# Kernel optimization log

Measured on AMD Instinct MI355X. Metric: run time of the kernel, lower is better.

## Reference

```python
import jax, jax.numpy as jnp
import numpy as np

S, B, D, H, DK, DFF, L, P = 128, 16, 512, 8, 64, 2048, 4, 4096


def setup_inputs() -> dict:
    key = jax.random.key(0)
    ks = jax.random.split(key, 10)
    def rn(k, shape, scale=0.02):
        return jax.random.normal(k, shape, jnp.float32) * scale
    return dict(
        x_seq=jax.random.normal(ks[0], (S, B, D), jnp.float32),
        w_query=rn(ks[1], (L, D, H * DK)),
        query_pos_bias=rn(ks[2], (L, H, DK)),
        key_pos_emb=rn(ks[3], (L, P, H, DK)),
        w_out=rn(ks[4], (L, D, D)), b_out=jnp.zeros((L, D), jnp.float32),
        ln1_g=jnp.ones((L, D), jnp.float32), ln1_b=jnp.zeros((L, D), jnp.float32),
        ln2_g=jnp.ones((L, D), jnp.float32), ln2_b=jnp.zeros((L, D), jnp.float32),
        w_ff1=rn(ks[5], (L, D, DFF)), b_ff1=jnp.zeros((L, DFF), jnp.float32),
        w_ff2=rn(ks[6], (L, DFF, D)), b_ff2=jnp.zeros((L, D), jnp.float32),
        norm_g=jnp.ones((D,), jnp.float32), norm_b=jnp.zeros((D,), jnp.float32),
        comb_w=jnp.ones((L + 1,), jnp.float32),
        w_key=rn(ks[7], (D, H * DK)), w_value=rn(ks[8], (D, H * DK)),
    )


def _layer_norm(x, g, b, eps=1e-5):
    mu = jnp.mean(x, -1, keepdims=True)
    var = jnp.mean((x - mu) ** 2, -1, keepdims=True)
    return (x - mu) * jax.lax.rsqrt(var + eps) * g + b


def reference(x_seq, w_query, query_pos_bias, key_pos_emb, w_out, b_out,
              ln1_g, ln1_b, ln2_g, ln2_b, w_ff1, b_ff1, w_ff2, b_ff2,
              norm_g, norm_b, comb_w, w_key, w_value):
    scale = 1.0 / jnp.sqrt(jnp.float32(DK))
    comb = jax.nn.softmax(comb_w)           # softmax over n_layers+1 weights
    jpos = jnp.arange(S)

    def step(carry, inp):
        mem_k, mem_v = carry                # [S, B, H, DK] growing KV memory stack
        x, t = inp                          # x: [B, D], t: scalar step index
        # valid memory slots are steps 0..t-1 (at t==0 attention is gated off below)
        valid = (jpos < jnp.maximum(t, 1))[:, None, None]   # [S,1,1]
        outs = [x]
        for l in range(L):
            # --- FeedbackAttention (pre-LN, relative key position embeddings) ---
            z = _layer_norm(x, ln1_g[l], ln1_b[l])
            q = (z @ w_query[l]).reshape(B, H, DK)
            # original: key_pos_embeddings[-t:]  ->  table index P - t + j for slot j
            kpe = jnp.take(key_pos_emb[l], jnp.clip(P - t + jpos, 0, P - 1), axis=0)  # [S,H,DK]
            ac = jnp.einsum('bhd,jbhd->jbh', q + query_pos_bias[l], mem_k)
            bd = jnp.einsum('bhd,jhd->jbh', q, kpe)
            scores = jnp.where(valid, (ac + bd) * scale, -1e9)
            attn = jax.nn.softmax(scores, axis=0)             # softmax over memory dim
            av = jnp.einsum('jbh,jbhd->bhd', attn, mem_v).reshape(B, D)
            x = jnp.where(t > 0, x + av @ w_out[l] + b_out[l], x)
            # --- FeedForward (pre-LN, ReLU) ---
            z = _layer_norm(x, ln2_g[l], ln2_b[l])
            x = x + jax.nn.relu(z @ w_ff1[l] + b_ff1[l]) @ w_ff2[l] + b_ff2[l]
            outs.append(x)
        # softmax-weighted combination of [input + layer outputs]
        mem = jnp.einsum('lbd,l->bd', jnp.stack(outs), comb)
        mem_k = mem_k.at[t].set((mem @ w_key).reshape(B, H, DK))
        mem_v = mem_v.at[t].set((mem @ w_value).reshape(B, H, DK))
        return (mem_k, mem_v), x

    mem0 = jnp.zeros((S, B, H, DK), x_seq.dtype)
    _, res = jax.lax.scan(jax.checkpoint(step), (mem0, mem0), (x_seq, jnp.arange(S)))
    return _layer_norm(res, norm_g, norm_b)
```

## Files before the change

kernel.cpp:

```cpp
#include <hip/hip_runtime.h>


#define S_ 128
#define B_ 16
#define D_ 512
#define H_ 8
#define DK_ 64
#define DFF_ 2048
#define L_ 4
#define P_ 4096

#define NBLK 128
#define NTHR 1024

struct FtkvParams {
  const float *x_seq, *w_query, *qpb, *kpe, *w_out, *b_out;
  const float *ln1_g, *ln1_b, *ln2_g, *ln2_b;
  const float *w_ff1, *b_ff1, *w_ff2, *b_ff2;
  const float *norm_g, *norm_b, *comb_w, *w_key, *w_value;
  float *out;
  float *dpart;
  float *dpart2;
  unsigned *memK;
  unsigned *memV;
  const uint4 *wqp;
  const uint4 *wop;
  const uint4 *w1p;
  const uint4 *w2p;
  const uint4 *wkp;
  const uint4 *wvp;
  unsigned int *bar;
};

__device__ __forceinline__ float cload(const float *p_) {
  return __hip_atomic_load(p_, __ATOMIC_RELAXED, __HIP_MEMORY_SCOPE_AGENT);
}
__device__ __forceinline__ void cstore(float *p_, float v) {
  __hip_atomic_store(p_, v, __ATOMIC_RELAXED, __HIP_MEMORY_SCOPE_AGENT);
}

__device__ __forceinline__ float waveRedSum(float v) {
#pragma unroll
  for (int off = 32; off; off >>= 1) v += __shfl_xor(v, off, 64);
  return v;
}
__device__ __forceinline__ float waveRedMax(float v) {
#pragma unroll
  for (int off = 32; off; off >>= 1) v = fmaxf(v, __shfl_xor(v, off, 64));
  return v;
}

#define UNPK(w, flo, fhi)                                     \
  float flo = __uint_as_float((unsigned)(w) << 16);           \
  float fhi = __uint_as_float((unsigned)(w) & 0xffff0000u);

__device__ __forceinline__ float dot8(const float *z, uint4 w) {
  UNPK(w.x, a0, a1); UNPK(w.y, b0, b1);
  UNPK(w.z, c0, c1); UNPK(w.w, d0, d1);
  return ((z[0] * a0 + z[1] * a1) + (z[2] * b0 + z[3] * b1)) +
         ((z[4] * c0 + z[5] * c1) + (z[6] * d0 + z[7] * d1));
}

__device__ __forceinline__ void gbarN(unsigned *arr, unsigned &epoch,
                                      unsigned n) {
  __syncthreads();
  const unsigned e = ++epoch;
  if (threadIdx.x == 0) {
    __hip_atomic_fetch_add(arr, 1u, __ATOMIC_RELAXED,
                           __HIP_MEMORY_SCOPE_AGENT);
    while (__hip_atomic_load(arr, __ATOMIC_RELAXED,
                             __HIP_MEMORY_SCOPE_AGENT) < e * n)
      __builtin_amdgcn_s_sleep(1);
  }
  __syncthreads();
}

__global__ void ftkv_init(unsigned *bar) {
  for (int i = threadIdx.x; i < 4096; i += 256) bar[i] = 0u;
}

__device__ __forceinline__ unsigned bf16rne(float x) {
  unsigned b = __float_as_uint(x);
  return (b + 0x7fffu + ((b >> 16) & 1u)) >> 16;
}

__global__ void ftkv_pack(const float *src, unsigned *dst, int K, int N) {
  int total = (K / 2) * N;
  int n4 = N * 4;
  for (int i = blockIdx.x * blockDim.x + threadIdx.x; i < total;
       i += gridDim.x * blockDim.x) {
    int k8 = i / n4, rem = i - k8 * n4;
    int col = rem >> 2, q = rem & 3;
    int r0 = 8 * k8 + 2 * q;
    dst[i] = bf16rne(src[(size_t)r0 * N + col]) |
             (bf16rne(src[(size_t)(r0 + 1) * N + col]) << 16);
  }
}

#define LNSTATS(val, mu_, rs_)                                             \
  {                                                                        \
    __syncthreads();                                                       \
    if (tid < 512) {                                                       \
      float _s1 = waveRedSum(val), _s2 = waveRedSum((val) * (val));        \
      if (lane == 0) { sRed[wid] = _s1; sRed[8 + wid] = _s2; }             \
    }                                                                      \
    __syncthreads();                                                       \
    if (tid == 0) {                                                        \
      float _a = 0.f, _c = 0.f;                                            \
      for (int _i = 0; _i < 8; ++_i) { _a += sRed[_i]; _c += sRed[8 + _i];}\
      float _mu = _a * (1.f / 512.f);                                      \
      float _var = _c * (1.f / 512.f) - _mu * _mu;                         \
      sRed[16] = _mu; sRed[17] = rsqrtf(_var + 1e-5f);                     \
    }                                                                      \
    __syncthreads();                                                       \
    mu_ = sRed[16]; rs_ = sRed[17];                                        \
  }

__global__ __launch_bounds__(NTHR, 4) void ftkv_main(FtkvParams p) {
  const int bid = blockIdx.x;
  const int tid = threadIdx.x;
  const int lane = tid & 63, wid = tid >> 6;
  const int g = bid >> 3;
  const int cs = bid & 7;

  __shared__ float sZ[512];
  __shared__ float sP[1024];
  __shared__ float sH[256];
  __shared__ float sQ[64], sQB[64], sS[128], sRed[20];

  unsigned *garr = p.bar + g * 32;
  unsigned gep = 0;

  float cw0 = p.comb_w[0], cw1 = p.comb_w[1], cw2 = p.comb_w[2],
        cw3 = p.comb_w[3], cw4 = p.comb_w[4];
  float cm = fmaxf(fmaxf(fmaxf(cw0, cw1), fmaxf(cw2, cw3)), cw4);
  float e0 = __expf(cw0 - cm), e1 = __expf(cw1 - cm), e2 = __expf(cw2 - cm),
        e3 = __expf(cw3 - cm), e4 = __expf(cw4 - cm);
  float einv = 1.0f / (e0 + e1 + e2 + e3 + e4);
  float comb0 = e0 * einv, comb1 = e1 * einv, comb2 = e2 * einv,
        comb3 = e3 * einv, comb4 = e4 * einv;

  float xr = 0.f, mr = 0.f;
  if (tid < 512) {
    xr = p.x_seq[g * D_ + tid];
    mr = comb0 * xr;
  }

  unsigned *memKb = p.memK + ((size_t)(g * H_ + cs)) * S_ * 32;
  unsigned *memVb = p.memV + ((size_t)(g * H_ + cs)) * S_ * 32;

  for (int t = 0; t < S_; ++t) {
    for (int l = 0; l < L_; ++l) {
      if (l > 0 && tid < 512) {
        float s = p.b_ff2[(l - 1) * D_ + tid];
#pragma unroll
        for (int c2 = 0; c2 < 8; ++c2)
          s += cload(&p.dpart2[((size_t)g * 8 + c2) * D_ + tid]);
        xr += s;
        const float cl = (l == 1) ? comb1 : (l == 2) ? comb2 : comb3;
        mr += cl * xr;
      }

      if (t > 0) {
        float mu, rs;
        LNSTATS(xr, mu, rs);
        if (tid < 512)
          sZ[tid] = (xr - mu) * rs * p.ln1_g[l * D_ + tid] +
                    p.ln1_b[l * D_ + tid];
        __syncthreads();
        {
          int d = tid & 63, ks = tid >> 6;
          const uint4 *wq = p.wqp + (size_t)l * 64 * 512 + cs * 64 + d;
          float acc = 0.f;
#pragma unroll
          for (int j = 0; j < 4; ++j) {
            int k8 = ks * 4 + j;
            acc += dot8(&sZ[8 * k8], wq[(size_t)k8 * 512]);
          }
          sP[tid] = acc;
        }
        __syncthreads();
        if (tid < 64) {
          float q = 0.f;
#pragma unroll
          for (int ks = 0; ks < 16; ++ks) q += sP[ks * 64 + tid];
          sQ[tid] = q;
          sQB[tid] = q + p.qpb[(l * H_ + cs) * 64 + tid];
        }
        __syncthreads();
        {
          int j = tid & 127, ds = tid >> 7;
          float acc = 0.f;
          if (j < t) {
            uint4 mku = ((const uint4 *)(memKb + (size_t)j * 32))[ds];
            const float4 *kp = (const float4 *)(p.kpe +
                (((size_t)l * P_ + (P_ - t + j)) * H_ + cs) * 64 + ds * 8);
            float4 b0 = kp[0], b1 = kp[1];
            UNPK(mku.x, k0, k1); UNPK(mku.y, k2, k3);
            UNPK(mku.z, k4, k5); UNPK(mku.w, k6, k7);
            const float *qb = &sQB[ds * 8], *qr = &sQ[ds * 8];
            acc = (qb[0] * k0 + qb[1] * k1 + qb[2] * k2 + qb[3] * k3) +
                  (qb[4] * k4 + qb[5] * k5 + qb[6] * k6 + qb[7] * k7) +
                  (qr[0] * b0.x + qr[1] * b0.y + qr[2] * b0.z + qr[3] * b0.w) +
                  (qr[4] * b1.x + qr[5] * b1.y + qr[6] * b1.z + qr[7] * b1.w);
          }
          sP[tid] = acc;
        }
        __syncthreads();
        if (tid < 128) {
          float sc = ((sP[tid] + sP[tid + 128]) + (sP[tid + 256] + sP[tid + 384])) +
                     ((sP[tid + 512] + sP[tid + 640]) + (sP[tid + 768] + sP[tid + 896]));
          sS[tid] = (tid < t) ? sc * 0.125f : -1e30f;
        }
        __syncthreads();
        if (tid < 64) {
          float m = waveRedMax(fmaxf(sS[tid], sS[tid + 64]));
          if (tid == 0) sRed[18] = m;
        }
        __syncthreads();
        if (tid < 128)
          sS[tid] = (tid < t) ? __expf(sS[tid] - sRed[18]) : 0.f;
        __syncthreads();
        if (tid < 64) {
          float s = waveRedSum(sS[tid] + sS[tid + 64]);
          if (tid == 0) sRed[19] = s;
        }
        __syncthreads();
        {
          int d = tid & 63, js = tid >> 6;
          int j0 = js * 8, j1 = (j0 + 8 < t) ? (j0 + 8) : t;
          float acc = 0.f;
          const ushort *mv = (const ushort *)memVb;
          for (int j = j0; j < j1; ++j) {
            float vv = __uint_as_float(((unsigned)mv[(size_t)j * 64 + d]) << 16);
            acc += sS[j] * vv;
          }
          sP[tid] = acc;
        }
        __syncthreads();
        if (tid < 64) {
          float a = 0.f;
#pragma unroll
          for (int js = 0; js < 16; ++js) a += sP[js * 64 + tid];
          sQ[tid] = a / sRed[19];
        }
        __syncthreads();
        {
          int col = tid & 511, ks = tid >> 9;
          const uint4 *wo = p.wop + (size_t)l * 64 * 512 + col;
          float acc = 0.f;
#pragma unroll
          for (int j = 0; j < 4; ++j) {
            int k8l = ks * 4 + j;
            acc += dot8(&sQ[8 * k8l], wo[(size_t)(cs * 8 + k8l) * 512]);
          }
          sP[tid] = acc;
        }
        __syncthreads();
        if (tid < 512)
          cstore(&p.dpart[((size_t)g * 8 + cs) * D_ + tid],
                 sP[tid] + sP[512 + tid]);
        gbarN(garr, gep, 8);
      }

      if (t > 0 && tid < 512) {
        float s = p.b_out[l * D_ + tid];
#pragma unroll
        for (int c2 = 0; c2 < 8; ++c2)
          s += cload(&p.dpart[((size_t)g * 8 + c2) * D_ + tid]);
        xr += s;
      }
      {
        float mu, rs;
        LNSTATS(xr, mu, rs);
        if (tid < 512)
          sZ[tid] = (xr - mu) * rs * p.ln2_g[l * D_ + tid] +
                    p.ln2_b[l * D_ + tid];
      }
      __syncthreads();
      {
        int c = tid & 255, ks = tid >> 8;
        const uint4 *w1 = p.w1p + (size_t)l * 64 * DFF_ + cs * 256 + c;
        float acc = 0.f;
#pragma unroll 8
        for (int j = 0; j < 16; ++j) {
          int k8 = ks * 16 + j;
          acc += dot8(&sZ[8 * k8], w1[(size_t)k8 * DFF_]);
        }
        sP[tid] = acc;
      }
      __syncthreads();
      if (tid < 256) {
        float h = ((sP[tid] + sP[256 + tid]) + (sP[512 + tid] + sP[768 + tid])) +
                  p.b_ff1[l * DFF_ + cs * 256 + tid];
        sH[tid] = fmaxf(h, 0.f);
      }
      __syncthreads();
      {
        int col = tid & 511, ks = tid >> 9;
        const uint4 *w2 = p.w2p + (size_t)l * 256 * 512 + col;
        float acc = 0.f;
#pragma unroll 8
        for (int j = 0; j < 16; ++j) {
          int k8l = ks * 16 + j;
          acc += dot8(&sH[8 * k8l], w2[(size_t)(cs * 32 + k8l) * 512]);
        }
        sP[tid] = acc;
      }
      __syncthreads();
      if (tid < 512)
        cstore(&p.dpart2[((size_t)g * 8 + cs) * D_ + tid],
               sP[tid] + sP[512 + tid]);
      gbarN(garr, gep, 8);
    }

    if (tid < 512) {
      float s = p.b_ff2[3 * D_ + tid];
#pragma unroll
      for (int c2 = 0; c2 < 8; ++c2)
        s += cload(&p.dpart2[((size_t)g * 8 + c2) * D_ + tid]);
      xr += s;
      mr += comb4 * xr;
      sZ[tid] = mr;
    }
    __syncthreads();
    {
      int kv = tid >> 9, r = tid & 511, d = r & 63, ks = r >> 6;
      const uint4 *w4 = (kv ? p.wvp : p.wkp) + cs * 64 + d;
      float acc = 0.f;
#pragma unroll
      for (int j = 0; j < 8; ++j) {
        int k8 = ks * 8 + j;
        acc += dot8(&sZ[8 * k8], w4[(size_t)k8 * 512]);
      }
      sP[tid] = acc;
    }
    __syncthreads();
    if (tid < 128) {
      int kv = tid >> 6, d = tid & 63;
      float v = 0.f;
#pragma unroll
      for (int ks = 0; ks < 8; ++ks) v += sP[kv * 512 + ks * 64 + d];
      sS[tid] = v;
    }
    __syncthreads();
    if (tid < 64) {
      int kv = tid >> 5, d2 = tid & 31;
      float lo = sS[kv * 64 + 2 * d2], hi = sS[kv * 64 + 2 * d2 + 1];
      unsigned pk = bf16rne(lo) | (bf16rne(hi) << 16);
      unsigned *dst = kv ? memVb : memKb;
      dst[(size_t)t * 32 + d2] = pk;
    }
    {
      float mu, rs;
      LNSTATS(xr, mu, rs);
      if (tid < 512 && (tid >> 6) == cs)
        p.out[((size_t)t * B_ + g) * D_ + tid] =
            (xr - mu) * rs * p.norm_g[tid] + p.norm_b[tid];
    }
    if (t + 1 < S_ && tid < 512) {
      xr = p.x_seq[((size_t)(t + 1) * B_ + g) * D_ + tid];
      mr = comb0 * xr;
    }
  }
}

extern "C" void kernel_launch(void *const *d_in, const int *in_sizes, int n_in,
                              void *d_out, int out_size, void *d_ws,
                              size_t ws_size, hipStream_t stream) {
  (void)in_sizes; (void)n_in; (void)out_size; (void)ws_size;

  FtkvParams p;
  p.x_seq  = (const float *)d_in[0];
  p.w_query = (const float *)d_in[1];
  p.qpb    = (const float *)d_in[2];
  p.kpe    = (const float *)d_in[3];
  p.w_out  = (const float *)d_in[4];
  p.b_out  = (const float *)d_in[5];
  p.ln1_g  = (const float *)d_in[6];
  p.ln1_b  = (const float *)d_in[7];
  p.ln2_g  = (const float *)d_in[8];
  p.ln2_b  = (const float *)d_in[9];
  p.w_ff1  = (const float *)d_in[10];
  p.b_ff1  = (const float *)d_in[11];
  p.w_ff2  = (const float *)d_in[12];
  p.b_ff2  = (const float *)d_in[13];
  p.norm_g = (const float *)d_in[14];
  p.norm_b = (const float *)d_in[15];
  p.comb_w = (const float *)d_in[16];
  p.w_key  = (const float *)d_in[17];
  p.w_value = (const float *)d_in[18];
  p.out = (float *)d_out;

  char *ws = (char *)d_ws;
  p.bar = (unsigned int *)ws;
  float *f = (float *)(ws + 16384);
  p.dpart  = f; f += B_ * 8 * D_;
  p.dpart2 = f; f += B_ * 8 * D_;
  unsigned *u = (unsigned *)f;
  p.memK = u; u += B_ * H_ * S_ * 32;
  p.memV = u; u += B_ * H_ * S_ * 32;
  unsigned *wqp = u; u += L_ * 256 * 512;
  unsigned *wop = u; u += L_ * 256 * 512;
  unsigned *w1p = u; u += L_ * 256 * DFF_;
  unsigned *w2p = u; u += L_ * 1024 * 512;
  unsigned *wkp = u; u += 256 * 512;
  unsigned *wvp = u; u += 256 * 512;
  p.wqp = (const uint4 *)wqp; p.wop = (const uint4 *)wop;
  p.w1p = (const uint4 *)w1p; p.w2p = (const uint4 *)w2p;
  p.wkp = (const uint4 *)wkp; p.wvp = (const uint4 *)wvp;

  ftkv_init<<<dim3(1), dim3(256), 0, stream>>>(p.bar);
  for (int l = 0; l < L_; ++l) {
    ftkv_pack<<<dim3(256), dim3(256), 0, stream>>>(
        p.w_query + (size_t)l * 512 * 512, wqp + (size_t)l * 256 * 512, 512, 512);
    ftkv_pack<<<dim3(256), dim3(256), 0, stream>>>(
// ... 11 lines not shown
```

Baseline: 14.26 ms.

## Assign block roles by XCC id so column slices share an XCD

Result: no change. 14.43 ms (+1.2%).

```diff
diff --git a/kernel.cpp b/kernel.cpp
--- a/kernel.cpp
+++ b/kernel.cpp
@@ -38,6 +38,9 @@
 __device__ __forceinline__ void cstore(float *p_, float v) {
   __hip_atomic_store(p_, v, __ATOMIC_RELAXED, __HIP_MEMORY_SCOPE_AGENT);
 }
+__device__ __forceinline__ unsigned aload(const unsigned *p_) {
+  return __hip_atomic_load(p_, __ATOMIC_RELAXED, __HIP_MEMORY_SCOPE_AGENT);
+}
 
 __device__ __forceinline__ float waveRedSum(float v) {
 #pragma unroll
@@ -117,16 +120,50 @@
   }
 
 __global__ __launch_bounds__(NTHR, 4) void ftkv_main(FtkvParams p) {
-  const int bid = blockIdx.x;
   const int tid = threadIdx.x;
   const int lane = tid & 63, wid = tid >> 6;
-  const int g = bid >> 3;
-  const int cs = bid & 7;
 
   __shared__ float sZ[512];
   __shared__ float sP[1024];
   __shared__ float sH[256];
   __shared__ float sQ[64], sQB[64], sS[128], sRed[20];
+  __shared__ int sAssign[2];
+
+  if (tid == 0) {
+    unsigned x;
+    asm volatile("s_getreg_b32 %0, hwreg(HW_REG_XCC_ID)" : "=s"(x));
+    x &= 7u;
+    unsigned *cnt = p.bar + 2048;
+    unsigned n = __hip_atomic_fetch_add(&cnt[x * 32], 1u, __ATOMIC_RELAXED,
+                                        __HIP_MEMORY_SCOPE_AGENT);
+    int mycs, myg;
+    if (n < 16u) {
+      mycs = (int)x;
+      myg = (int)n;
+    } else {
+      for (;;) {
+        unsigned s = 0;
+        for (int i = 0; i < 8; ++i) s += aload(&cnt[i * 32]);
+        if (s >= (unsigned)NBLK) break;
+        __builtin_amdgcn_s_sleep(8);
+      }
+      unsigned e = __hip_atomic_fetch_add(&cnt[256], 1u, __ATOMIC_RELAXED,
+                                          __HIP_MEMORY_SCOPE_AGENT);
+      mycs = 0; myg = 0;
+      for (int c = 0; c < 8; ++c) {
+        unsigned cc = aload(&cnt[c * 32]);
+        unsigned used = cc < 16u ? cc : 16u;
+        unsigned u = 16u - used;
+        if (e < u) { mycs = c; myg = (int)(used + e); break; }
+        e -= u;
+      }
+    }
+    sAssign[0] = mycs;
+    sAssign[1] = myg;
+  }
+  __syncthreads();
+  const int cs = sAssign[0];
+  const int g = sAssign[1];
 
   unsigned *garr = p.bar + g * 32;
   unsigned gep = 0;
```

## Interleave two batch groups per block with split arrive/wait barriers

Applied to the files above, without the earlier changes.

New measurement: 26.99 ms. 1.89x slower.

```diff
diff --git a/kernel.cpp b/kernel.cpp
--- a/kernel.cpp
+++ b/kernel.cpp
@@ -10,7 +10,7 @@
 #define L_ 4
 #define P_ 4096
 
-#define NBLK 128
+#define NBLK 64
 #define NTHR 1024
 
 struct FtkvParams {
@@ -61,15 +61,17 @@
          ((z[4] * c0 + z[5] * c1) + (z[6] * d0 + z[7] * d1));
 }
 
-__device__ __forceinline__ void gbarN(unsigned *arr, unsigned &epoch,
-                                      unsigned n) {
-  __syncthreads();
-  const unsigned e = ++epoch;
-  if (threadIdx.x == 0) {
+__device__ __forceinline__ void arrive(unsigned *arr, unsigned &ep) {
+  __syncthreads();
+  if (threadIdx.x == 0)
     __hip_atomic_fetch_add(arr, 1u, __ATOMIC_RELAXED,
                            __HIP_MEMORY_SCOPE_AGENT);
+  ++ep;
+}
+__device__ __forceinline__ void waitbar(unsigned *arr, unsigned ep) {
+  if (threadIdx.x == 0) {
     while (__hip_atomic_load(arr, __ATOMIC_RELAXED,
-                             __HIP_MEMORY_SCOPE_AGENT) < e * n)
+                             __HIP_MEMORY_SCOPE_AGENT) < ep * 8u)
       __builtin_amdgcn_s_sleep(1);
   }
   __syncthreads();
@@ -97,39 +99,247 @@
   }
 }
 
-#define LNSTATS(val, mu_, rs_)                                             \
-  {                                                                        \
-    __syncthreads();                                                       \
-    if (tid < 512) {                                                       \
-      float _s1 = waveRedSum(val), _s2 = waveRedSum((val) * (val));        \
-      if (lane == 0) { sRed[wid] = _s1; sRed[8 + wid] = _s2; }             \
-    }                                                                      \
-    __syncthreads();                                                       \
-    if (tid == 0) {                                                        \
-      float _a = 0.f, _c = 0.f;                                            \
-      for (int _i = 0; _i < 8; ++_i) { _a += sRed[_i]; _c += sRed[8 + _i];}\
-      float _mu = _a * (1.f / 512.f);                                      \
-      float _var = _c * (1.f / 512.f) - _mu * _mu;                         \
-      sRed[16] = _mu; sRed[17] = rsqrtf(_var + 1e-5f);                     \
-    }                                                                      \
-    __syncthreads();                                                       \
-    mu_ = sRed[16]; rs_ = sRed[17];                                        \
-  }
+__device__ __forceinline__ void lnstats(int tid, int lane, int wid, float v,
+                                        float *sRed, float &mu, float &rs) {
+  __syncthreads();
+  if (tid < 512) {
+    float s1 = waveRedSum(v), s2 = waveRedSum(v * v);
+    if (lane == 0) { sRed[wid] = s1; sRed[8 + wid] = s2; }
+  }
+  __syncthreads();
+  float a = 0.f, c = 0.f;
+#pragma unroll
+  for (int i = 0; i < 8; ++i) { a += sRed[i]; c += sRed[8 + i]; }
+  mu = a * (1.f / 512.f);
+  float var = c * (1.f / 512.f) - mu * mu;
+  rs = rsqrtf(var + 1e-5f);
+}
+
+struct Smem {
+  float sZ[512];
+  float sP[1024];
+  float sH[256];
+  float sQ[64], sQB[64], sS[128], sRed[20];
+};
+
+__device__ __forceinline__ void bodyA(const FtkvParams &p, Smem &sm, int tid,
+                                      int lane, int wid, int t, int l, int g,
+                                      int cs, float xr, unsigned *memKb,
+                                      unsigned *memVb) {
+  float mu, rs;
+  lnstats(tid, lane, wid, xr, sm.sRed, mu, rs);
+  if (tid < 512)
+    sm.sZ[tid] = (xr - mu) * rs * p.ln1_g[l * D_ + tid] +
+                 p.ln1_b[l * D_ + tid];
+  __syncthreads();
+  {
+    int d = tid & 63, ks = tid >> 6;
+    const uint4 *wq = p.wqp + (size_t)l * 64 * 512 + cs * 64 + d;
+    float acc = 0.f;
+#pragma unroll
+    for (int j = 0; j < 4; ++j) {
+      int k8 = ks * 4 + j;
+      acc += dot8(&sm.sZ[8 * k8], wq[(size_t)k8 * 512]);
+    }
+    sm.sP[tid] = acc;
+  }
+  __syncthreads();
+  if (tid < 64) {
+    float q = 0.f;
+#pragma unroll
+    for (int ks = 0; ks < 16; ++ks) q += sm.sP[ks * 64 + tid];
+    sm.sQ[tid] = q;
+    sm.sQB[tid] = q + p.qpb[(l * H_ + cs) * 64 + tid];
+  }
+  __syncthreads();
+  {
+    int j = tid & 127, ds = tid >> 7;
+    float acc = 0.f;
+    if (j < t) {
+      uint4 mku = ((const uint4 *)(memKb + (size_t)j * 32))[ds];
+      const float4 *kp = (const float4 *)(p.kpe +
+          (((size_t)l * P_ + (P_ - t + j)) * H_ + cs) * 64 + ds * 8);
+      float4 b0 = kp[0], b1 = kp[1];
+      UNPK(mku.x, k0, k1); UNPK(mku.y, k2, k3);
+      UNPK(mku.z, k4, k5); UNPK(mku.w, k6, k7);
+      const float *qb = &sm.sQB[ds * 8], *qr = &sm.sQ[ds * 8];
+      acc = (qb[0] * k0 + qb[1] * k1 + qb[2] * k2 + qb[3] * k3) +
+            (qb[4] * k4 + qb[5] * k5 + qb[6] * k6 + qb[7] * k7) +
+            (qr[0] * b0.x + qr[1] * b0.y + qr[2] * b0.z + qr[3] * b0.w) +
+            (qr[4] * b1.x + qr[5] * b1.y + qr[6] * b1.z + qr[7] * b1.w);
+    }
+    sm.sP[tid] = acc;
+  }
+  __syncthreads();
+  if (tid < 128) {
+    float sc =
+        ((sm.sP[tid] + sm.sP[tid + 128]) + (sm.sP[tid + 256] + sm.sP[tid + 384])) +
+        ((sm.sP[tid + 512] + sm.sP[tid + 640]) + (sm.sP[tid + 768] + sm.sP[tid + 896]));
+    sm.sS[tid] = (tid < t) ? sc * 0.125f : -1e30f;
+  }
+  __syncthreads();
+  if (tid < 64) {
+    float m = waveRedMax(fmaxf(sm.sS[tid], sm.sS[tid + 64]));
+    if (tid == 0) sm.sRed[18] = m;
+  }
+  __syncthreads();
+  if (tid < 128)
+    sm.sS[tid] = (tid < t) ? __expf(sm.sS[tid] - sm.sRed[18]) : 0.f;
+  __syncthreads();
+  if (tid < 64) {
+    float s = waveRedSum(sm.sS[tid] + sm.sS[tid + 64]);
+    if (tid == 0) sm.sRed[19] = s;
+  }
+  __syncthreads();
+  {
+    int d = tid & 63, js = tid >> 6;
+    int j0 = js * 8, j1 = (j0 + 8 < t) ? (j0 + 8) : t;
+    float acc = 0.f;
+    const ushort *mv = (const ushort *)memVb;
+    for (int j = j0; j < j1; ++j) {
+      float vv = __uint_as_float(((unsigned)mv[(size_t)j * 64 + d]) << 16);
+      acc += sm.sS[j] * vv;
+    }
+    sm.sP[tid] = acc;
+  }
+  __syncthreads();
+  if (tid < 64) {
+    float a = 0.f;
+#pragma unroll
+    for (int js = 0; js < 16; ++js) a += sm.sP[js * 64 + tid];
+    sm.sQ[tid] = a / sm.sRed[19];
+  }
+  __syncthreads();
+  {
+    int col = tid & 511, ks = tid >> 9;
+    const uint4 *wo = p.wop + (size_t)l * 64 * 512 + col;
+    float acc = 0.f;
+#pragma unroll
+    for (int j = 0; j < 4; ++j) {
+      int k8l = ks * 4 + j;
+      acc += dot8(&sm.sQ[8 * k8l], wo[(size_t)(cs * 8 + k8l) * 512]);
+    }
+    sm.sP[tid] = acc;
+  }
+  __syncthreads();
+  if (tid < 512)
+    cstore(&p.dpart[((size_t)g * 8 + cs) * D_ + tid],
+           sm.sP[tid] + sm.sP[512 + tid]);
+}
+
+__device__ __forceinline__ void bodyB(const FtkvParams &p, Smem &sm, int tid,
+                                      int lane, int wid, int l, int g, int cs,
+                                      float xr) {
+  float mu, rs;
+  lnstats(tid, lane, wid, xr, sm.sRed, mu, rs);
+  if (tid < 512)
+    sm.sZ[tid] = (xr - mu) * rs * p.ln2_g[l * D_ + tid] +
+                 p.ln2_b[l * D_ + tid];
+  __syncthreads();
+  {
+    int c = tid & 255, ks = tid >> 8;
+    const uint4 *w1 = p.w1p + (size_t)l * 64 * DFF_ + cs * 256 + c;
+    float acc = 0.f;
+#pragma unroll 8
+    for (int j = 0; j < 16; ++j) {
+      int k8 = ks * 16 + j;
+      acc += dot8(&sm.sZ[8 * k8], w1[(size_t)k8 * DFF_]);
+    }
+    sm.sP[tid] = acc;
+  }
+  __syncthreads();
+  if (tid < 256) {
+    float h = ((sm.sP[tid] + sm.sP[256 + tid]) +
+               (sm.sP[512 + tid] + sm.sP[768 + tid])) +
+              p.b_ff1[l * DFF_ + cs * 256 + tid];
+    sm.sH[tid] = fmaxf(h, 0.f);
+  }
+  __syncthreads();
+  {
+    int col = tid & 511, ks = tid >> 9;
+    const uint4 *w2 = p.w2p + (size_t)l * 256 * 512 + col;
+    float acc = 0.f;
+#pragma unroll 8
+    for (int j = 0; j < 16; ++j) {
+      int k8l = ks * 16 + j;
+      acc += dot8(&sm.sH[8 * k8l], w2[(size_t)(cs * 32 + k8l) * 512]);
+    }
+    sm.sP[tid] = acc;
+  }
+  __syncthreads();
+  if (tid < 512)
+    cstore(&p.dpart2[((size_t)g * 8 + cs) * D_ + tid],
+           sm.sP[tid] + sm.sP[512 + tid]);
+}
+
+__device__ __forceinline__ void bodyE(const FtkvParams &p, Smem &sm, int tid,
+                                      int lane, int wid, int t, int g, int cs,
+                                      float &xr, float &mr, float comb0,
+                                      float comb4, unsigned *memKb,
+                                      unsigned *memVb) {
+  if (tid < 512) {
+    float s = p.b_ff2[3 * D_ + tid];
+#pragma unroll
+    for (int c2 = 0; c2 < 8; ++c2)
+      s += cload(&p.dpart2[((size_t)g * 8 + c2) * D_ + tid]);
+    xr += s;
+    mr += comb4 * xr;
+    sm.sZ[tid] = mr;
+  }
+  __syncthreads();
+  {
+    int kv = tid >> 9, r = tid & 511, d = r & 63, ks = r >> 6;
+    const uint4 *w4 = (kv ? p.wvp : p.wkp) + cs * 64 + d;
+    float acc = 0.f;
+#pragma unroll
+    for (int j = 0; j < 8; ++j) {
+      int k8 = ks * 8 + j;
+      acc += dot8(&sm.sZ[8 * k8], w4[(size_t)k8 * 512]);
+    }
+    sm.sP[tid] = acc;
+  }
+  __syncthreads();
+  if (tid < 128) {
+    int kv = tid >> 6, d = tid & 63;
+    float v = 0.f;
+#pragma unroll
+    for (int ks = 0; ks < 8; ++ks) v += sm.sP[kv * 512 + ks * 64 + d];
+    sm.sS[tid] = v;
+  }
+  __syncthreads();
+  if (tid < 64) {
+    int kv = tid >> 5, d2 = tid & 31;
+    float lo = sm.sS[kv * 64 + 2 * d2], hi = sm.sS[kv * 64 + 2 * d2 + 1];
+    unsigned pk = bf16rne(lo) | (bf16rne(hi) << 16);
+    unsigned *dst = kv ? memVb : memKb;
+    dst[(size_t)t * 32 + d2] = pk;
+  }
+  {
+    float mu, rs;
+    lnstats(tid, lane, wid, xr, sm.sRed, mu, rs);
+    if (tid < 512 && (tid >> 6) == cs)
+      p.out[((size_t)t * B_ + g) * D_ + tid] =
+          (xr - mu) * rs * p.norm_g[tid] + p.norm_b[tid];
+  }
+  if (t + 1 < S_ && tid < 512) {
+    xr = p.x_seq[((size_t)(t + 1) * B_ + g) * D_ + tid];
+    mr = comb0 * xr;
+  }
+}
 
 __global__ __launch_bounds__(NTHR, 4) void ftkv_main(FtkvParams p) {
   const int bid = blockIdx.x;
   const int tid = threadIdx.x;
   const int lane = tid & 63, wid = tid >> 6;
-  const int g = bid >> 3;
+  const int gp = bid >> 3;
   const int cs = bid & 7;
 
-  __shared__ float sZ[512];
-  __shared__ float sP[1024];
-  __shared__ float sH[256];
-  __shared__ float sQ[64], sQB[64], sS[128], sRed[20];
-
-  unsigned *garr = p.bar + g * 32;
-  unsigned gep = 0;
+  __shared__ Smem sm;
+
+  const int gA = gp, gB = gp + 8;
+  unsigned *arrA = p.bar + gA * 32;
+  unsigned *arrB = p.bar + gB * 32;
+  unsigned epA = 0, epB = 0;
 
   float cw0 = p.comb_w[0], cw1 = p.comb_w[1], cw2 = p.comb_w[2],
         cw3 = p.comb_w[3], cw4 = p.comb_w[4];
@@ -140,228 +350,102 @@
   float comb0 = e0 * einv, comb1 = e1 * einv, comb2 = e2 * einv,
         comb3 = e3 * einv, comb4 = e4 * einv;
 
-  float xr = 0.f, mr = 0.f;
+  float xrA = 0.f, mrA = 0.f, xrB = 0.f, mrB = 0.f;
   if (tid < 512) {
-    xr = p.x_seq[g * D_ + tid];
-    mr = comb0 * xr;
-  }
-
-  unsigned *memKb = p.memK + ((size_t)(g * H_ + cs)) * S_ * 32;
-  unsigned *memVb = p.memV + ((size_t)(g * H_ + cs)) * S_ * 32;
+    xrA = p.x_seq[gA * D_ + tid];
+    mrA = comb0 * xrA;
+    xrB = p.x_seq[gB * D_ + tid];
+    mrB = comb0 * xrB;
+  }
+
+  unsigned *memKbA = p.memK + ((size_t)(gA * H_ + cs)) * S_ * 32;
+  unsigned *memVbA = p.memV + ((size_t)(gA * H_ + cs)) * S_ * 32;
+  unsigned *memKbB = p.memK + ((size_t)(gB * H_ + cs)) * S_ * 32;
+  unsigned *memVbB = p.memV + ((size_t)(gB * H_ + cs)) * S_ * 32;
 
   for (int t = 0; t < S_; ++t) {
     for (int l = 0; l < L_; ++l) {
-      if (l > 0 && tid < 512) {
-        float s = p.b_ff2[(l - 1) * D_ + tid];
-#pragma unroll
-        for (int c2 = 0; c2 < 8; ++c2)
-          s += cload(&p.dpart2[((size_t)g * 8 + c2) * D_ + tid]);
-        xr += s;
-        const float cl = (l == 1) ? comb1 : (l == 2) ? comb2 : comb3;
-        mr += cl * xr;
+      const float cl = (l == 1) ? comb1 : (l == 2) ? comb2 : comb3;
+
+      if (t > 0) {
+        waitbar(arrA, epA);
+        if (l > 0 && tid < 512) {
+          float s = p.b_ff2[(l - 1) * D_ + tid];
+#pragma unroll
+          for (int c2 = 0; c2 < 8; ++c2)
+            s += cload(&p.dpart2[((size_t)gA * 8 + c2) * D_ + tid]);
+          xrA += s;
+          mrA += cl * xrA;
+        }
+        bodyA(p, sm, tid, lane, wid, t, l, gA, cs, xrA, memKbA, memVbA);
+        arrive(arrA, epA);
+
+        waitbar(arrB, epB);
+        if (l > 0 && tid < 512) {
+          float s = p.b_ff2[(l - 1) * D_ + tid];
+#pragma unroll
+          for (int c2 = 0; c2 < 8; ++c2)
+            s += cload(&p.dpart2[((size_t)gB * 8 + c2) * D_ + tid]);
+          xrB += s;
+          mrB += cl * xrB;
+        }
+        bodyA(p, sm, tid, lane, wid, t, l, gB, cs, xrB, memKbB, memVbB);
+        arrive(arrB, epB);
+
+        waitbar(arrA, epA);
+        if (tid < 512) {
+          float s = p.b_out[l * D_ + tid];
+#pragma unroll
+          for (int c2 = 0; c2 < 8; ++c2)
+            s += cload(&p.dpart[((size_t)gA * 8 + c2) * D_ + tid]);
+          xrA += s;
+        }
+        bodyB(p, sm, tid, lane, wid, l, gA, cs, xrA);
+        arrive(arrA, epA);
+
+        waitbar(arrB, epB);
+        if (tid < 512) {
+          float s = p.b_out[l * D_ + tid];
+#pragma unroll
+          for (int c2 = 0; c2 < 8; ++c2)
+            s += cload(&p.dpart[((size_t)gB * 8 + c2) * D_ + tid]);
+          xrB += s;
+        }
+        bodyB(p, sm, tid, lane, wid, l, gB, cs, xrB);
+        arrive(arrB, epB);
+      } else {
+        waitbar(arrA, epA);
+        if (l > 0 && tid < 512) {
+          float s = p.b_ff2[(l - 1) * D_ + tid];
+#pragma unroll
+          for (int c2 = 0; c2 < 8; ++c2)
+            s += cload(&p.dpart2[((size_t)gA * 8 + c2) * D_ + tid]);
+          xrA += s;
+          mrA += cl * xrA;
+        }
+        bodyB(p, sm, tid, lane, wid, l, gA, cs, xrA);
+        arrive(arrA, epA);
+
+        waitbar(arrB, epB);
+        if (l > 0 && tid < 512) {
+          float s = p.b_ff2[(l - 1) * D_ + tid];
+#pragma unroll
+          for (int c2 = 0; c2 < 8; ++c2)
+            s += cload(&p.dpart2[((size_t)gB * 8 + c2) * D_ + tid]);
+          xrB += s;
+          mrB += cl * xrB;
+        }
+        bodyB(p, sm, tid, lane, wid, l, gB, cs, xrB);
+        arrive(arrB, epB);
       }
-
-      if (t > 0) {
-        float mu, rs;
-        LNSTATS(xr, mu, rs);
-        if (tid < 512)
-          sZ[tid] = (xr - mu) * rs * p.ln1_g[l * D_ + tid] +
-                    p.ln1_b[l * D_ + tid];
-        __syncthreads();
-        {
-          int d = tid & 63, ks = tid >> 6;
-          const uint4 *wq = p.wqp + (size_t)l * 64 * 512 + cs * 64 + d;
-          float acc = 0.f;
-#pragma unroll
-          for (int j = 0; j < 4; ++j) {
-            int k8 = ks * 4 + j;
-            acc += dot8(&sZ[8 * k8], wq[(size_t)k8 * 512]);
-          }
-          sP[tid] = acc;
-        }
-        __syncthreads();
-        if (tid < 64) {
-          float q = 0.f;
-#pragma unroll
-          for (int ks = 0; ks < 16; ++ks) q += sP[ks * 64 + tid];
-          sQ[tid] = q;
-          sQB[tid] = q + p.qpb[(l * H_ + cs) * 64 + tid];
-        }
-        __syncthreads();
-        {
-          int j = tid & 127, ds = tid >> 7;
-          float acc = 0.f;
-          if (j < t) {
-            uint4 mku = ((const uint4 *)(memKb + (size_t)j * 32))[ds];
-            const float4 *kp = (const float4 *)(p.kpe +
-                (((size_t)l * P_ + (P_ - t + j)) * H_ + cs) * 64 + ds * 8);
-            float4 b0 = kp[0], b1 = kp[1];
-            UNPK(mku.x, k0, k1); UNPK(mku.y, k2, k3);
-            UNPK(mku.z, k4, k5); UNPK(mku.w, k6, k7);
-            const float *qb = &sQB[ds * 8], *qr = &sQ[ds * 8];
-            acc = (qb[0] * k0 + qb[1] * k1 + qb[2] * k2 + qb[3] * k3) +
-                  (qb[4] * k4 + qb[5] * k5 + qb[6] * k6 + qb[7] * k7) +
-                  (qr[0] * b0.x + qr[1] * b0.y + qr[2] * b0.z + qr[3] * b0.w) +
-                  (qr[4] * b1.x + qr[5] * b1.y + qr[6] * b1.z + qr[7] * b1.w);
-          }
-          sP[tid] = acc;
-        }
-        __syncthreads();
-        if (tid < 128) {
-          float sc = ((sP[tid] + sP[tid + 128]) + (sP[tid + 256] + sP[tid + 384])) +
-                     ((sP[tid + 512] + sP[tid + 640]) + (sP[tid + 768] + sP[tid + 896]));
-          sS[tid] = (tid < t) ? sc * 0.125f : -1e30f;
-        }
-        __syncthreads();
-        if (tid < 64) {
-          float m = waveRedMax(fmaxf(sS[tid], sS[tid + 64]));
-          if (tid == 0) sRed[18] = m;
-        }
-        __syncthreads();
-        if (tid < 128)
-          sS[tid] = (tid < t) ? __expf(sS[tid] - sRed[18]) : 0.f;
-        __syncthreads();
-        if (tid < 64) {
-          float s = waveRedSum(sS[tid] + sS[tid + 64]);
-          if (tid == 0) sRed[19] = s;
-        }
-        __syncthreads();
-        {
-          int d = tid & 63, js = tid >> 6;
-          int j0 = js * 8, j1 = (j0 + 8 < t) ? (j0 + 8) : t;
-          float acc = 0.f;
-          const ushort *mv = (const ushort *)memVb;
-          for (int j = j0; j < j1; ++j) {
-            float vv = __uint_as_float(((unsigned)mv[(size_t)j * 64 + d]) << 16);
-            acc += sS[j] * vv;
-          }
-          sP[tid] = acc;
-        }
-        __syncthreads();
-        if (tid < 64) {
-          float a = 0.f;
-#pragma unroll
-          for (int js = 0; js < 16; ++js) a += sP[js * 64 + tid];
-          sQ[tid] = a / sRed[19];
-        }
-        __syncthreads();
-        {
-          int col = tid & 511, ks = tid >> 9;
-          const uint4 *wo = p.wop + (size_t)l * 64 * 512 + col;
-          float acc = 0.f;
-#pragma unroll
-          for (int j = 0; j < 4; ++j) {
-            int k8l = ks * 4 + j;
-            acc += dot8(&sQ[8 * k8l], wo[(size_t)(cs * 8 + k8l) * 512]);
-          }
-          sP[tid] = acc;
-        }
-        __syncthreads();
-        if (tid < 512)
-          cstore(&p.dpart[((size_t)g * 8 + cs) * D_ + tid],
-                 sP[tid] + sP[512 + tid]);
-        gbarN(garr, gep, 8);
-      }
-
-      if (t > 0 && tid < 512) {
-        float s = p.b_out[l * D_ + tid];
-#pragma unroll
-        for (int c2 = 0; c2 < 8; ++c2)
-          s += cload(&p.dpart[((size_t)g * 8 + c2) * D_ + tid]);
-        xr += s;
-      }
-      {
-        float mu, rs;
-        LNSTATS(xr, mu, rs);
-        if (tid < 512)
-          sZ[tid] = (xr - mu) * rs * p.ln2_g[l * D_ + tid] +
-                    p.ln2_b[l * D_ + tid];
-      }
-      __syncthreads();
-      {
-        int c = tid & 255, ks = tid >> 8;
-        const uint4 *w1 = p.w1p + (size_t)l * 64 * DFF_ + cs * 256 + c;
-        float acc = 0.f;
-#pragma unroll 8
-        for (int j = 0; j < 16; ++j) {
-          int k8 = ks * 16 + j;
-          acc += dot8(&sZ[8 * k8], w1[(size_t)k8 * DFF_]);
-        }
-        sP[tid] = acc;
-      }
-      __syncthreads();
-      if (tid < 256) {
-        float h = ((sP[tid] + sP[256 + tid]) + (sP[512 + tid] + sP[768 + tid])) +
-                  p.b_ff1[l * DFF_ + cs * 256 + tid];
-        sH[tid] = fmaxf(h, 0.f);
-      }
-      __syncthreads();
-      {
-        int col = tid & 511, ks = tid >> 9;
-        const uint4 *w2 = p.w2p + (size_t)l * 256 * 512 + col;
-        float acc = 0.f;
-#pragma unroll 8
-        for (int j = 0; j < 16; ++j) {
-          int k8l = ks * 16 + j;
-          acc += dot8(&sH[8 * k8l], w2[(size_t)(cs * 32 + k8l) * 512]);
-        }
-        sP[tid] = acc;
-      }
-      __syncthreads();
-      if (tid < 512)
-        cstore(&p.dpart2[((size_t)g * 8 + cs) * D_ + tid],
-               sP[tid] + sP[512 + tid]);
-      gbarN(garr, gep, 8);
-    }
-
-    if (tid < 512) {
-      float s = p.b_ff2[3 * D_ + tid];
-#pragma unroll
-      for (int c2 = 0; c2 < 8; ++c2)
-        s += cload(&p.dpart2[((size_t)g * 8 + c2) * D_ + tid]);
-      xr += s;
-      mr += comb4 * xr;
-      sZ[tid] = mr;
-    }
-    __syncthreads();
-    {
-      int kv = tid >> 9, r = tid & 511, d = r & 63, ks = r >> 6;
-      const uint4 *w4 = (kv ? p.wvp : p.wkp) + cs * 64 + d;
-      float acc = 0.f;
-#pragma unroll
-      for (int j = 0; j < 8; ++j) {
-        int k8 = ks * 8 + j;
-        acc += dot8(&sZ[8 * k8], w4[(size_t)k8 * 512]);
-      }
-      sP[tid] = acc;
-    }
-    __syncthreads();
-    if (tid < 128) {
-      int kv = tid >> 6, d = tid & 63;
-      float v = 0.f;
-#pragma unroll
-      for (int ks = 0; ks < 8; ++ks) v += sP[kv * 512 + ks * 64 + d];
-      sS[tid] = v;
-    }
-    __syncthreads();
-    if (tid < 64) {
-      int kv = tid >> 5, d2 = tid & 31;
-      float lo = sS[kv * 64 + 2 * d2], hi = sS[kv * 64 + 2 * d2 + 1];
-      unsigned pk = bf16rne(lo) | (bf16rne(hi) << 16);
-      unsigned *dst = kv ? memVb : memKb;
-      dst[(size_t)t * 32 + d2] = pk;
-    }
-    {
-      float mu, rs;
-      LNSTATS(xr, mu, rs);
-      if (tid < 512 && (tid >> 6) == cs)
-        p.out[((size_t)t * B_ + g) * D_ + tid] =
-            (xr - mu) * rs * p.norm_g[tid] + p.norm_b[tid];
-    }
-    if (t + 1 < S_ && tid < 512) {
-      xr = p.x_seq[((size_t)(t + 1) * B_ + g) * D_ + tid];
-      mr = comb0 * xr;
-    }
+    }
+
+    waitbar(arrA, epA);
+    bodyE(p, sm, tid, lane, wid, t, gA, cs, xrA, mrA, comb0, comb4, memKbA,
+          memVbA);
+    waitbar(arrB, epB);
+    bodyE(p, sm, tid, lane, wid, t, gB, cs, xrB, mrB, comb0, comb4, memKbB,
+          memVbB);
   }
 }
 
```

## Prefetch weights into registers before LN barriers and use LDS-only barriers

Applied to the files above, without the earlier changes.

New measurement: 11.66 ms. 18.2% less time.

```diff
diff --git a/kernel.cpp b/kernel.cpp
--- a/kernel.cpp
+++ b/kernel.cpp
@@ -50,6 +50,11 @@
   return v;
 }
 
+__device__ __forceinline__ void lbar() {
+  asm volatile("s_waitcnt lgkmcnt(0)" ::: "memory");
+  __builtin_amdgcn_s_barrier();
+}
+
 #define UNPK(w, flo, fhi)                                     \
   float flo = __uint_as_float((unsigned)(w) << 16);           \
   float fhi = __uint_as_float((unsigned)(w) & 0xffff0000u);
@@ -61,15 +66,14 @@
          ((z[4] * c0 + z[5] * c1) + (z[6] * d0 + z[7] * d1));
 }
 
-__device__ __forceinline__ void gbarN(unsigned *arr, unsigned &epoch,
-                                      unsigned n) {
+__device__ __forceinline__ void gbarN(unsigned *arr, unsigned &epoch) {
   __syncthreads();
   const unsigned e = ++epoch;
   if (threadIdx.x == 0) {
     __hip_atomic_fetch_add(arr, 1u, __ATOMIC_RELAXED,
                            __HIP_MEMORY_SCOPE_AGENT);
     while (__hip_atomic_load(arr, __ATOMIC_RELAXED,
-                             __HIP_MEMORY_SCOPE_AGENT) < e * n)
+                             __HIP_MEMORY_SCOPE_AGENT) < e * 8u)
       __builtin_amdgcn_s_sleep(1);
   }
   __syncthreads();
@@ -97,24 +101,28 @@
   }
 }
 
-#define LNSTATS(val, mu_, rs_)                                             \
-  {                                                                        \
-    __syncthreads();                                                       \
-    if (tid < 512) {                                                       \
-      float _s1 = waveRedSum(val), _s2 = waveRedSum((val) * (val));        \
-      if (lane == 0) { sRed[wid] = _s1; sRed[8 + wid] = _s2; }             \
-    }                                                                      \
-    __syncthreads();                                                       \
-    if (tid == 0) {                                                        \
-      float _a = 0.f, _c = 0.f;                                            \
-      for (int _i = 0; _i < 8; ++_i) { _a += sRed[_i]; _c += sRed[8 + _i];}\
-      float _mu = _a * (1.f / 512.f);                                      \
-      float _var = _c * (1.f / 512.f) - _mu * _mu;                         \
-      sRed[16] = _mu; sRed[17] = rsqrtf(_var + 1e-5f);                     \
-    }                                                                      \
-    __syncthreads();                                                       \
-    mu_ = sRed[16]; rs_ = sRed[17];                                        \
-  }
+struct Smem {
+  float sZ[512];
+  float sP[1024];
+  float sH[256];
+  float sQ[64], sQB[64], sS[128], sRed[24];
+};
+
+__device__ __forceinline__ void lnstats(int tid, int lane, int wid, float v,
+                                        float *sRed, float &mu, float &rs) {
+  lbar();
+  if (tid < 512) {
+    float s1 = waveRedSum(v), s2 = waveRedSum(v * v);
+    if (lane == 0) { sRed[wid] = s1; sRed[8 + wid] = s2; }
+  }
+  lbar();
+  float a = 0.f, c = 0.f;
+#pragma unroll
+  for (int i = 0; i < 8; ++i) { a += sRed[i]; c += sRed[8 + i]; }
+  mu = a * (1.f / 512.f);
+  float var = c * (1.f / 512.f) - mu * mu;
+  rs = rsqrtf(var + 1e-5f);
+}
 
 __global__ __launch_bounds__(NTHR, 4) void ftkv_main(FtkvParams p) {
   const int bid = blockIdx.x;
@@ -123,10 +131,7 @@
   const int g = bid >> 3;
   const int cs = bid & 7;
 
-  __shared__ float sZ[512];
-  __shared__ float sP[1024];
-  __shared__ float sH[256];
-  __shared__ float sQ[64], sQB[64], sS[128], sRed[20];
+  __shared__ Smem sm;
 
   unsigned *garr = p.bar + g * 32;
   unsigned gep = 0;
@@ -149,218 +154,242 @@
   unsigned *memKb = p.memK + ((size_t)(g * H_ + cs)) * S_ * 32;
   unsigned *memVb = p.memV + ((size_t)(g * H_ + cs)) * S_ * 32;
 
+  const int d6 = tid & 63, ks16 = tid >> 6;
+  const int j7 = tid & 127, ds8 = tid >> 7;
+  const int col9 = tid & 511, ks2 = tid >> 9;
+  const int c8 = tid & 255, ksb = tid >> 8;
+
   for (int t = 0; t < S_; ++t) {
     for (int l = 0; l < L_; ++l) {
+      const float cl = (l == 1) ? comb1 : (l == 2) ? comb2 : comb3;
+
       if (l > 0 && tid < 512) {
         float s = p.b_ff2[(l - 1) * D_ + tid];
 #pragma unroll
         for (int c2 = 0; c2 < 8; ++c2)
           s += cload(&p.dpart2[((size_t)g * 8 + c2) * D_ + tid]);
         xr += s;
-        const float cl = (l == 1) ? comb1 : (l == 2) ? comb2 : comb3;
         mr += cl * xr;
       }
 
       if (t > 0) {
+        uint4 wq[4], wo[4];
+        {
+          const uint4 *wqp = p.wqp + (size_t)l * 64 * 512 + cs * 64 + d6;
+#pragma unroll
+          for (int j = 0; j < 4; ++j) wq[j] = wqp[(size_t)(ks16 * 4 + j) * 512];
+          const uint4 *wop = p.wop + (size_t)l * 64 * 512 + col9;
+#pragma unroll
+          for (int j = 0; j < 4; ++j)
+            wo[j] = wop[(size_t)(cs * 8 + ks2 * 4 + j) * 512];
+        }
+        uint4 mku = ((const uint4 *)(memKb + (size_t)j7 * 32))[ds8];
+        int kidx = P_ - t + j7;
+        kidx = kidx < 0 ? 0 : (kidx > P_ - 1 ? P_ - 1 : kidx);
+        const float4 *kpp = (const float4 *)(p.kpe +
+            (((size_t)l * P_ + kidx) * H_ + cs) * 64 + ds8 * 8);
+        float4 kp0 = kpp[0], kp1 = kpp[1];
+        unsigned mvp[8];
+        {
+#pragma unroll
+          for (int jj = 0; jj < 8; ++jj)
+            mvp[jj] = memVb[(size_t)(ks16 * 8 + jj) * 32 + (d6 >> 1)];
+        }
+
         float mu, rs;
-        LNSTATS(xr, mu, rs);
+        lnstats(tid, lane, wid, xr, sm.sRed, mu, rs);
         if (tid < 512)
-          sZ[tid] = (xr - mu) * rs * p.ln1_g[l * D_ + tid] +
-                    p.ln1_b[l * D_ + tid];
-        __syncthreads();
-        {
-          int d = tid & 63, ks = tid >> 6;
-          const uint4 *wq = p.wqp + (size_t)l * 64 * 512 + cs * 64 + d;
+          sm.sZ[tid] = (xr - mu) * rs * p.ln1_g[l * D_ + tid] +
+                       p.ln1_b[l * D_ + tid];
+        lbar();
+        {
           float acc = 0.f;
 #pragma unroll
-          for (int j = 0; j < 4; ++j) {
-            int k8 = ks * 4 + j;
-            acc += dot8(&sZ[8 * k8], wq[(size_t)k8 * 512]);
-          }
-          sP[tid] = acc;
-        }
-        __syncthreads();
+          for (int j = 0; j < 4; ++j)
+            acc += dot8(&sm.sZ[8 * (ks16 * 4 + j)], wq[j]);
+          sm.sP[tid] = acc;
+        }
+        lbar();
         if (tid < 64) {
           float q = 0.f;
 #pragma unroll
-          for (int ks = 0; ks < 16; ++ks) q += sP[ks * 64 + tid];
-          sQ[tid] = q;
-          sQB[tid] = q + p.qpb[(l * H_ + cs) * 64 + tid];
-        }
-        __syncthreads();
-        {
-          int j = tid & 127, ds = tid >> 7;
+          for (int ks = 0; ks < 16; ++ks) q += sm.sP[ks * 64 + tid];
+          sm.sQ[tid] = q;
+          sm.sQB[tid] = q + p.qpb[(l * H_ + cs) * 64 + tid];
+        }
+        lbar();
+        {
+          UNPK(mku.x, k0, k1); UNPK(mku.y, k2, k3);
+          UNPK(mku.z, k4, k5); UNPK(mku.w, k6, k7);
+          const float *qb = &sm.sQB[ds8 * 8], *qr = &sm.sQ[ds8 * 8];
+          float acc =
+              (qb[0] * k0 + qb[1] * k1 + qb[2] * k2 + qb[3] * k3) +
+              (qb[4] * k4 + qb[5] * k5 + qb[6] * k6 + qb[7] * k7) +
+              (qr[0] * kp0.x + qr[1] * kp0.y + qr[2] * kp0.z + qr[3] * kp0.w) +
+              (qr[4] * kp1.x + qr[5] * kp1.y + qr[6] * kp1.z + qr[7] * kp1.w);
+          sm.sP[tid] = acc;
+        }
+        lbar();
+        if (tid < 128) {
+          float sc = ((sm.sP[tid] + sm.sP[tid + 128]) +
+                      (sm.sP[tid + 256] + sm.sP[tid + 384])) +
+                     ((sm.sP[tid + 512] + sm.sP[tid + 640]) +
+                      (sm.sP[tid + 768] + sm.sP[tid + 896]));
+          sm.sS[tid] = (tid < t) ? sc * 0.125f : -1e30f;
+        }
+        lbar();
+        if (tid < 64) {
+          float a0 = sm.sS[tid], a1 = sm.sS[tid + 64];
+          float m = waveRedMax(fmaxf(a0, a1));
+          float ee0 = __expf(a0 - m), ee1 = __expf(a1 - m);
+          float s = waveRedSum(ee0 + ee1);
+          sm.sS[tid] = ee0;
+          sm.sS[64 + tid] = ee1;
+          if (tid == 0) sm.sRed[19] = s;
+        }
+        lbar();
+        {
           float acc = 0.f;
-          if (j < t) {
-            uint4 mku = ((const uint4 *)(memKb + (size_t)j * 32))[ds];
-            const float4 *kp = (const float4 *)(p.kpe +
-                (((size_t)l * P_ + (P_ - t + j)) * H_ + cs) * 64 + ds * 8);
-            float4 b0 = kp[0], b1 = kp[1];
-            UNPK(mku.x, k0, k1); UNPK(mku.y, k2, k3);
-            UNPK(mku.z, k4, k5); UNPK(mku.w, k6, k7);
-            const float *qb = &sQB[ds * 8], *qr = &sQ[ds * 8];
-            acc = (qb[0] * k0 + qb[1] * k1 + qb[2] * k2 + qb[3] * k3) +
-                  (qb[4] * k4 + qb[5] * k5 + qb[6] * k6 + qb[7] * k7) +
-                  (qr[0] * b0.x + qr[1] * b0.y + qr[2] * b0.z + qr[3] * b0.w) +
-                  (qr[4] * b1.x + qr[5] * b1.y + qr[6] * b1.z + qr[7] * b1.w);
+#pragma unroll
+          for (int jj = 0; jj < 8; ++jj) {
+            UNPK(mvp[jj], v0, v1);
+            float vv = (d6 & 1) ? v1 : v0;
+            acc += sm.sS[ks16 * 8 + jj] * vv;
           }
-          sP[tid] = acc;
-        }
-        __syncthreads();
-        if (tid < 128) {
-          float sc = ((sP[tid] + sP[tid + 128]) + (sP[tid + 256] + sP[tid + 384])) +
-                     ((sP[tid + 512] + sP[tid + 640]) + (sP[tid + 768] + sP[tid + 896]));
-          sS[tid] = (tid < t) ? sc * 0.125f : -1e30f;
-        }
-        __syncthreads();
-        if (tid < 64) {
-          float m = waveRedMax(fmaxf(sS[tid], sS[tid + 64]));
-          if (tid == 0) sRed[18] = m;
-        }
-        __syncthreads();
-        if (tid < 128)
-          sS[tid] = (tid < t) ? __expf(sS[tid] - sRed[18]) : 0.f;
-        __syncthreads();
-        if (tid < 64) {
-          float s = waveRedSum(sS[tid] + sS[tid + 64]);
-          if (tid == 0) sRed[19] = s;
-        }
-        __syncthreads();
-        {
-          int d = tid & 63, js = tid >> 6;
-          int j0 = js * 8, j1 = (j0 + 8 < t) ? (j0 + 8) : t;
-          float acc = 0.f;
-          const ushort *mv = (const ushort *)memVb;
-          for (int j = j0; j < j1; ++j) {
-            float vv = __uint_as_float(((unsigned)mv[(size_t)j * 64 + d]) << 16);
-            acc += sS[j] * vv;
-          }
-          sP[tid] = acc;
-        }
-        __syncthreads();
+          sm.sP[tid] = acc;
+        }
+        lbar();
         if (tid < 64) {
           float a = 0.f;
 #pragma unroll
-          for (int js = 0; js < 16; ++js) a += sP[js * 64 + tid];
-          sQ[tid] = a / sRed[19];
-        }
-        __syncthreads();
-        {
-          int col = tid & 511, ks = tid >> 9;
-          const uint4 *wo = p.wop + (size_t)l * 64 * 512 + col;
+          for (int js = 0; js < 16; ++js) a += sm.sP[js * 64 + tid];
+          sm.sQ[tid] = a / sm.sRed[19];
+        }
+        lbar();
+        {
           float acc = 0.f;
 #pragma unroll
-          for (int j = 0; j < 4; ++j) {
-            int k8l = ks * 4 + j;
-            acc += dot8(&sQ[8 * k8l], wo[(size_t)(cs * 8 + k8l) * 512]);
-          }
-          sP[tid] = acc;
-        }
-        __syncthreads();
+          for (int j = 0; j < 4; ++j)
+            acc += dot8(&sm.sQ[8 * (ks2 * 4 + j)], wo[j]);
+          sm.sP[tid] = acc;
+        }
+        lbar();
         if (tid < 512)
           cstore(&p.dpart[((size_t)g * 8 + cs) * D_ + tid],
-                 sP[tid] + sP[512 + tid]);
-        gbarN(garr, gep, 8);
-      }
-
-      if (t > 0 && tid < 512) {
-        float s = p.b_out[l * D_ + tid];
+                 sm.sP[tid] + sm.sP[512 + tid]);
+        gbarN(garr, gep);
+
+        if (tid < 512) {
+          float s = p.b_out[l * D_ + tid];
+#pragma unroll
+          for (int c2 = 0; c2 < 8; ++c2)
+            s += cload(&p.dpart[((size_t)g * 8 + c2) * D_ + tid]);
+          xr += s;
+        }
+      }
+
+      {
+        uint4 w1r[16];
+        {
+          const uint4 *w1 = p.w1p + (size_t)l * 64 * DFF_ + cs * 256 + c8;
+#pragma unroll
+          for (int j = 0; j < 16; ++j)
+            w1r[j] = w1[(size_t)(ksb * 16 + j) * DFF_];
+        }
+        float mu, rs;
+        lnstats(tid, lane, wid, xr, sm.sRed, mu, rs);
+        if (tid < 512)
+          sm.sZ[tid] = (xr - mu) * rs * p.ln2_g[l * D_ + tid] +
+                       p.ln2_b[l * D_ + tid];
+        lbar();
+        {
+          float acc = 0.f;
+#pragma unroll
+          for (int j = 0; j < 16; ++j)
+            acc += dot8(&sm.sZ[8 * (ksb * 16 + j)], w1r[j]);
+          sm.sP[tid] = acc;
+        }
+        uint4 w2r[16];
+        {
+          const uint4 *w2 = p.w2p + (size_t)l * 256 * 512 + col9;
+#pragma unroll
+          for (int j = 0; j < 16; ++j)
+            w2r[j] = w2[(size_t)(cs * 32 + ks2 * 16 + j) * 512];
+        }
+        lbar();
+        if (tid < 256) {
+          float h = ((sm.sP[tid] + sm.sP[256 + tid]) +
+                     (sm.sP[512 + tid] + sm.sP[768 + tid])) +
+                    p.b_ff1[l * DFF_ + cs * 256 + tid];
+          sm.sH[tid] = fmaxf(h, 0.f);
+        }
+        lbar();
+        {
+          float acc = 0.f;
+#pragma unroll
+          for (int j = 0; j < 16; ++j)
+            acc += dot8(&sm.sH[8 * (ks2 * 16 + j)], w2r[j]);
+          sm.sP[tid] = acc;
+        }
+        lbar();
+        if (tid < 512)
+          cstore(&p.dpart2[((size_t)g * 8 + cs) * D_ + tid],
+                 sm.sP[tid] + sm.sP[512 + tid]);
+      }
+      gbarN(garr, gep);
+    }
+
+    {
+      const int kv = tid >> 9, rE = tid & 511, dE = rE & 63, ks8 = rE >> 6;
+      uint4 wkv[8];
+      {
+        const uint4 *w4 = (kv ? p.wvp : p.wkp) + cs * 64 + dE;
+#pragma unroll
+        for (int j = 0; j < 8; ++j) wkv[j] = w4[(size_t)(ks8 * 8 + j) * 512];
+      }
+      if (tid < 512) {
+        float s = p.b_ff2[3 * D_ + tid];
 #pragma unroll
         for (int c2 = 0; c2 < 8; ++c2)
-          s += cload(&p.dpart[((size_t)g * 8 + c2) * D_ + tid]);
+          s += cload(&p.dpart2[((size_t)g * 8 + c2) * D_ + tid]);
         xr += s;
-      }
+        mr += comb4 * xr;
+        sm.sZ[tid] = mr;
+      }
+      lbar();
       {
-        float mu, rs;
-        LNSTATS(xr, mu, rs);
-        if (tid < 512)
-          sZ[tid] = (xr - mu) * rs * p.ln2_g[l * D_ + tid] +
-                    p.ln2_b[l * D_ + tid];
+        float acc = 0.f;
+#pragma unroll
+        for (int j = 0; j < 8; ++j)
+          acc += dot8(&sm.sZ[8 * (ks8 * 8 + j)], wkv[j]);
+        sm.sP[tid] = acc;
+      }
+      lbar();
+      if (tid < 128) {
+        int kv2 = tid >> 6, d = tid & 63;
+        float v = 0.f;
+#pragma unroll
+        for (int ks = 0; ks < 8; ++ks) v += sm.sP[kv2 * 512 + ks * 64 + d];
+        sm.sS[tid] = v;
+      }
+      lbar();
+      if (tid < 64) {
+        int kv2 = tid >> 5, d2 = tid & 31;
+        float lo = sm.sS[kv2 * 64 + 2 * d2], hi = sm.sS[kv2 * 64 + 2 * d2 + 1];
+        unsigned pk = bf16rne(lo) | (bf16rne(hi) << 16);
+        unsigned *dst = kv2 ? memVb : memKb;
+        dst[(size_t)t * 32 + d2] = pk;
       }
       __syncthreads();
-      {
-        int c = tid & 255, ks = tid >> 8;
-        const uint4 *w1 = p.w1p + (size_t)l * 64 * DFF_ + cs * 256 + c;
-        float acc = 0.f;
-#pragma unroll 8
-        for (int j = 0; j < 16; ++j) {
-          int k8 = ks * 16 + j;
-          acc += dot8(&sZ[8 * k8], w1[(size_t)k8 * DFF_]);
-        }
-        sP[tid] = acc;
-      }
-      __syncthreads();
-      if (tid < 256) {
-        float h = ((sP[tid] + sP[256 + tid]) + (sP[512 + tid] + sP[768 + tid])) +
-                  p.b_ff1[l * DFF_ + cs * 256 + tid];
-        sH[tid] = fmaxf(h, 0.f);
-      }
-      __syncthreads();
-      {
-        int col = tid & 511, ks = tid >> 9;
-        const uint4 *w2 = p.w2p + (size_t)l * 256 * 512 + col;
-        float acc = 0.f;
-#pragma unroll 8
-        for (int j = 0; j < 16; ++j) {
-          int k8l = ks * 16 + j;
-          acc += dot8(&sH[8 * k8l], w2[(size_t)(cs * 32 + k8l) * 512]);
-        }
-        sP[tid] = acc;
-      }
-      __syncthreads();
-      if (tid < 512)
-        cstore(&p.dpart2[((size_t)g * 8 + cs) * D_ + tid],
-               sP[tid] + sP[512 + tid]);
-      gbarN(garr, gep, 8);
-    }
-
-    if (tid < 512) {
-      float s = p.b_ff2[3 * D_ + tid];
-#pragma unroll
-      for (int c2 = 0; c2 < 8; ++c2)
-        s += cload(&p.dpart2[((size_t)g * 8 + c2) * D_ + tid]);
-      xr += s;
-      mr += comb4 * xr;
-      sZ[tid] = mr;
-    }
-    __syncthreads();
-    {
-      int kv = tid >> 9, r = tid & 511, d = r & 63, ks = r >> 6;
-      const uint4 *w4 = (kv ? p.wvp : p.wkp) + cs * 64 + d;
-      float acc = 0.f;
-#pragma unroll
-      for (int j = 0; j < 8; ++j) {
-        int k8 = ks * 8 + j;
-        acc += dot8(&sZ[8 * k8], w4[(size_t)k8 * 512]);
-      }
-      sP[tid] = acc;
-    }
-    __syncthreads();
-    if (tid < 128) {
-      int kv = tid >> 6, d = tid & 63;
-      float v = 0.f;
-#pragma unroll
-      for (int ks = 0; ks < 8; ++ks) v += sP[kv * 512 + ks * 64 + d];
-      sS[tid] = v;
-    }
-    __syncthreads();
-    if (tid < 64) {
-      int kv = tid >> 5, d2 = tid & 31;
-      float lo = sS[kv * 64 + 2 * d2], hi = sS[kv * 64 + 2 * d2 + 1];
-      unsigned pk = bf16rne(lo) | (bf16rne(hi) << 16);
-      unsigned *dst = kv ? memVb : memKb;
-      dst[(size_t)t * 32 + d2] = pk;
-    }
-    {
       float mu, rs;
-      LNSTATS(xr, mu, rs);
+      lnstats(tid, lane, wid, xr, sm.sRed, mu, rs);
       if (tid < 512 && (tid >> 6) == cs)
         p.out[((size_t)t * B_ + g) * D_ + tid] =
             (xr - mu) * rs * p.norm_g[tid] + p.norm_b[tid];
-    }
-    if (t + 1 < S_ && tid < 512) {
-      xr = p.x_seq[((size_t)(t + 1) * B_ + g) * D_ + tid];
-      mr = comb0 * xr;
+      if (t + 1 < S_ && tid < 512) {
+        xr = p.x_seq[((size_t)(t + 1) * B_ + g) * D_ + tid];
+        mr = comb0 * xr;
+      }
     }
   }
 }
```
